# Performance work log

Measured on AMD Instinct MI355X. Metric: run time of the kernel, lower is better.

Reference implementation:

```python
import jax, jax.numpy as jnp
import numpy as np
from math import comb

G, NPG, D = 32, 128, 128   # graphs, nodes-per-graph, hidden dim
N = G * NPG                # 4096 nodes per side
E = 65536                  # edges per side (avg degree 16)
K = 6                      # Bernstein order (bern_k)
S, DCONV, DTR = 16, 4, 8   # mamba d_state, d_conv, dt_rank
HE = 27
SIGMAS = [1.0, 10.0, 100.0, 1000.0, 10000.0]


def _leaky(x, s=0.02):
    return jnp.where(x >= 0, x, s * x)


def _bnorm(x, g, b, eps=1e-5):
    m = jnp.mean(x, axis=0)
    v = jnp.var(x, axis=0)
    return (x - m) * jax.lax.rsqrt(v + eps) * g + b


def _bern_prop(x, src, dst, w, temp):
    # BernNet Bern_prop: Bernstein polynomial of sym-normalized Laplacian with weights relu(temp)
    n = x.shape[0]
    temp = jax.nn.relu(temp)
    deg = jax.ops.segment_sum(w, src, num_segments=n)
    dinv = jnp.where(deg > 0, 1.0 / jnp.sqrt(deg + 1e-12), 0.0)
    nw = (w * dinv[src] * dinv[dst])[:, None]
    adj = lambda v: jax.ops.segment_sum(nw * v[src], dst, num_segments=n)
    tmps = [x]
    xv = x
    for _ in range(K):
        xv = xv + adj(xv)          # (2I - L) v = v + A_norm v
        tmps.append(xv)
    out = (comb(K, 0) / 2 ** K) * temp[0] * tmps[K]
    for i in range(K):
        v = tmps[K - i - 1]
        for _ in range(i + 1):
            v = v - adj(v)         # L v = v - A_norm v
        out = out + (comb(K, i + 1) / 2 ** K) * temp[i + 1] * v
    return out


def _mamba(h, in_w, conv_w, conv_b, xproj_w, dt_w, dt_b, A_log, Dp, out_w):
    # Mamba block, d_model=D, expand=1 (d_inner=D), d_state=S, d_conv=DCONV
    Bb, L, _ = h.shape
    xq, z = jnp.split(h @ in_w, 2, axis=-1)             # [B,L,D] each
    xp = jnp.pad(xq, ((0, 0), (DCONV - 1, 0), (0, 0)))  # causal depthwise conv
    xc = conv_b + sum(xp[:, k:k + L, :] * conv_w[:, k] for k in range(DCONV))
    xc = jax.nn.silu(xc)
    dbl = xc @ xproj_w                                  # [B,L,DTR+2S]
    dt = jax.nn.softplus(dbl[..., :DTR] @ dt_w + dt_b)  # [B,L,D]
    Bm = dbl[..., DTR:DTR + S]
    Cm = dbl[..., DTR + S:]
    A = -jnp.exp(A_log)                                 # [D,S]
    dA = jnp.exp(dt[..., None] * A)                     # [B,L,D,S]
    dBx = dt[..., None] * Bm[:, :, None, :] * xc[..., None]

    def step(hs, ins):
        dA_t, dBx_t, C_t = ins
        hs = dA_t * hs + dBx_t
        return hs, jnp.einsum('bds,bs->bd', hs, C_t)

    h0 = jnp.zeros((Bb, D, S), h.dtype)
    _, ys = jax.lax.scan(step, h0, (jnp.swapaxes(dA, 0, 1),
                                    jnp.swapaxes(dBx, 0, 1),
                                    jnp.swapaxes(Cm, 0, 1)))
    y = jnp.swapaxes(ys, 0, 1) + xc * Dp
    return (y * jax.nn.silu(z)) @ out_w


def _xattn(q, k, v, mask):
    a = mask * (q @ k.T) - 1000.0 * (1.0 - mask)
    return jax.nn.softmax(a, axis=1) @ v


def setup_inputs():
    key = jax.random.key(0)
    ks = jax.random.split(key, 32)
    f = jnp.float32
    nrm = lambda k, shp, sc=1.0: jax.random.normal(k, shp, dtype=f) * sc
    h_lig = nrm(ks[0], (N, D), 0.5)
    h_rec = nrm(ks[1], (N, D), 0.5)
    x_lig = nrm(ks[2], (N, 3))
    x_rec = nrm(ks[3], (N, 3))
    he_1 = jax.random.uniform(ks[4], (E, HE), dtype=f)
    he_2 = jax.random.uniform(ks[5], (E, HE), dtype=f)
    g = (jnp.arange(E) // (E // G)).astype(jnp.int32)
    src1 = g * NPG + jax.random.randint(ks[6], (E,), 0, NPG, dtype=jnp.int32)
    dst1 = g * NPG + jax.random.randint(ks[7], (E,), 0, NPG, dtype=jnp.int32)
    src2 = g * NPG + jax.random.randint(ks[8], (E,), 0, NPG, dtype=jnp.int32)
    dst2 = g * NPG + jax.random.randint(ks[9], (E,), 0, NPG, dtype=jnp.int32)
    edge_index_1 = jnp.stack([src1, dst1])
    edge_index_2 = jnp.stack([src2, dst2])
    batch = (jnp.arange(N) // NPG).astype(jnp.int32)
    rng = np.random.default_rng(0)
    def mkperm(src):
        # lexsort([deg + noise, batch]) with batch as primary key
        deg = np.bincount(np.asarray(src), minlength=N).astype(np.float32)
        return jnp.asarray(np.lexsort((deg + rng.random(N).astype(np.float32),
                                       np.asarray(batch))).astype(np.int32))
    perm_1 = mkperm(src1)
    perm_2 = mkperm(src2)
    p = {}
    p['emlp_w1'] = nrm(ks[10], (32, D), 0.1)
    p['emlp_b1'] = jnp.zeros((D,), f)
    p['emlp_bn_g'] = jnp.ones((D,), f)
    p['emlp_bn_b'] = jnp.zeros((D,), f)
    p['emlp_w2'] = nrm(ks[11], (D, 1), 0.1)
    p['emlp_b2'] = jnp.zeros((1,), f)
    p['bern_temp'] = jnp.ones((K + 1,), f)
    p['m_in_w'] = nrm(ks[12], (D, 2 * D), 0.05)
    p['m_conv_w'] = nrm(ks[13], (D, DCONV), 0.2)
    p['m_conv_b'] = jnp.zeros((D,), f)
    p['m_xproj_w'] = nrm(ks[14], (D, DTR + 2 * S), 0.05)
    p['m_dt_w'] = nrm(ks[15], (DTR, D), 0.2)
    p['m_dt_b'] = jnp.full((D,), -4.0, f)
    p['m_A_log'] = jnp.log(jnp.broadcast_to(jnp.arange(1, S + 1, dtype=f), (D, S)))
    p['m_D'] = jnp.ones((D,), f)
    p['m_out_w'] = nrm(ks[16], (D, D), 0.05)
    p['q_w'] = nrm(ks[17], (D, D), 0.05)
    p['k_w'] = nrm(ks[18], (D, D), 0.05)
    p['v_w'] = nrm(ks[19], (D, D), 0.05)
    p['bn1_g'] = jnp.ones((D,), f)
    p['bn1_b'] = jnp.zeros((D,), f)
    p['bn2_g'] = jnp.ones((D,), f)
    p['bn2_b'] = jnp.zeros((D,), f)
    p['ff_w1'] = nrm(ks[20], (D, 2 * D), 0.05)
    p['ff_b1'] = jnp.zeros((2 * D,), f)
    p['ff_w2'] = nrm(ks[21], (2 * D, D), 0.05)
    p['ff_b2'] = jnp.zeros((D,), f)
    return dict(h_lig=h_lig, h_rec=h_rec, x_lig=x_lig, x_rec=x_rec,
                he_1=he_1, he_2=he_2, **p,
                edge_index_1=edge_index_1, edge_index_2=edge_index_2,
                batch_1=batch, batch_2=batch, perm_1=perm_1, perm_2=perm_2)


def reference(h_lig, h_rec, x_lig, x_rec, he_1, he_2,
              emlp_w1, emlp_b1, emlp_bn_g, emlp_bn_b, emlp_w2, emlp_b2,
              bern_temp, m_in_w, m_conv_w, m_conv_b, m_xproj_w, m_dt_w,
              m_dt_b, m_A_log, m_D, m_out_w, q_w, k_w, v_w,
              bn1_g, bn1_b, bn2_g, bn2_b, ff_w1, ff_b1, ff_w2, ff_b2,
              edge_index_1, edge_index_2, batch_1, batch_2, perm_1, perm_2):

    def side(h, x, he, ei, perm):
        src, dst = ei[0], ei[1]
        d2 = jnp.sum((x[src] - x[dst]) ** 2, axis=1, keepdims=True)
        ew = jnp.concatenate([jnp.exp(-d2 / s) for s in SIGMAS], axis=1)  # [E,5]
        t = _leaky(jnp.concatenate([ew, he], axis=1) @ emlp_w1 + emlp_b1)
        t = _bnorm(t, emlp_bn_g, emlp_bn_b)
        w = jax.nn.relu(t @ emlp_w2 + emlp_b2)[:, 0]                      # [E]
        h_local = _bern_prop(h, src, dst, w, bern_temp)
        inv = jnp.argsort(perm)
        hd = h[perm].reshape(G, NPG, D)   # uniform graph sizes -> exact dense batch
        ha = _mamba(hd, m_in_w, m_conv_w, m_conv_b, m_xproj_w, m_dt_w,
                    m_dt_b, m_A_log, m_D, m_out_w).reshape(N, D)[inv]
        return _bnorm(h + h_local + ha, bn1_g, bn1_b)

    hl = side(h_lig, x_lig, he_1, edge_index_1, perm_1)
    hr = side(h_rec, x_rec, he_2, edge_index_2, perm_2)
    mask = (batch_1[:, None] == batch_2[None, :]).astype(hl.dtype)
    cl = _xattn(_leaky(hl @ q_w), _leaky(hr @ k_w), hr @ v_w, mask)
    cr = _xattn(_leaky(hr @ q_w), _leaky(hl @ k_w), hl @ v_w, mask.T)
    hl = hl + cl
    hr = hr + cr
    ff = lambda h: jax.nn.relu(h @ ff_w1 + ff_b1) @ ff_w2 + ff_b2
    hl = _bnorm(hl + ff(hl), bn2_g, bn2_b)
    hr = _bnorm(hr + ff(hr), bn2_g, bn2_b)
    return hl, hr
```

## Files before the change

### kernel.cpp

```cpp
#include <hip/hip_runtime.h>
#include <math.h>

#define G_    32
#define NPG_  128
#define D_    128
#define N_    4096
#define E_    65536
#define ND_   (N_*D_)

#define W_OFF     0
#define DEG_OFF   65536
#define STATS_OFF 69632
#define BUF0      71680
#define HL_OFF    (BUF0 + 0*ND_)
#define HA_OFF    (BUF0 + 1*ND_)
#define X1_OFF    (BUF0 + 2*ND_)
#define HMID_OFF  (BUF0 + 3*ND_)
#define XC_OFF    (BUF0 + 4*ND_)
#define DTB_OFF   (BUF0 + 5*ND_)
#define YB_OFF    (BUF0 + 6*ND_)
#define XZ_OFF    (BUF0 + 7*ND_)
#define DBL_OFF   (BUF0 + 9*ND_)
#define SS_       ((size_t)(DBL_OFF + N_*40))

__device__ __forceinline__ float leakyf(float x){ return x >= 0.f ? x : 0.02f*x; }
__device__ __forceinline__ float siluf (float x){ return x / (1.f + expf(-x)); }

__device__ __forceinline__ void edge_feat(const float* __restrict__ x,
                                          const float* __restrict__ he,
                                          const int* __restrict__ ei,
                                          int e, float* feat, int& sN, int& dN)
{
  sN = ei[e]; dN = ei[E_ + e];
  float dx = x[sN*3+0]-x[dN*3+0];
  float dy = x[sN*3+1]-x[dN*3+1];
  float dz = x[sN*3+2]-x[dN*3+2];
  float d2 = dx*dx + dy*dy + dz*dz;
  feat[0] = expf(-d2/1.f);
  feat[1] = expf(-d2/10.f);
  feat[2] = expf(-d2/100.f);
  feat[3] = expf(-d2/1000.f);
  feat[4] = expf(-d2/10000.f);
#pragma unroll
  for (int j = 0; j < 27; ++j) feat[5+j] = he[(size_t)e*27 + j];
}

__global__ __launch_bounds__(256)
void edge_stats_kernel(const float* __restrict__ xl, const float* __restrict__ xr,
                       const float* __restrict__ hel, const float* __restrict__ her,
                       const int* __restrict__ ei1, const int* __restrict__ ei2,
                       const float* __restrict__ w1, const float* __restrict__ b1,
                       float* __restrict__ ws)
{
  int side = blockIdx.y;
  const float* x  = side ? xr  : xl;
  const float* he = side ? her : hel;
  const int*   ei = side ? ei2 : ei1;
  float* stats = ws + (size_t)side*SS_ + STATS_OFF;
  __shared__ float featl[256*36];
  __shared__ float csum[2][128], cssq[2][128];
  int tid = threadIdx.x;
  {
    int sN, dN; float feat[32];
    edge_feat(x, he, ei, blockIdx.x*256 + tid, feat, sN, dN);
#pragma unroll
    for (int j4 = 0; j4 < 8; ++j4)
      *(float4*)&featl[tid*36 + j4*4] = *(float4*)&feat[j4*4];
  }
  int c = tid & 127, hh = tid >> 7;
  float w1c[32];
#pragma unroll
  for (int j = 0; j < 32; ++j) w1c[j] = w1[j*128 + c];
  float b1c = b1[c];
  __syncthreads();
  float s1 = 0.f, s2 = 0.f;
  for (int e = 0; e < 128; ++e) {
    const float* f = &featl[(hh*128 + e)*36];
    float acc = b1c;
#pragma unroll
    for (int j4 = 0; j4 < 8; ++j4) {
      float4 f4 = *(const float4*)&f[j4*4];
      acc += f4.x*w1c[j4*4] + f4.y*w1c[j4*4+1] + f4.z*w1c[j4*4+2] + f4.w*w1c[j4*4+3];
    }
    float t = leakyf(acc);
    s1 += t; s2 += t*t;
  }
  csum[hh][c] = s1; cssq[hh][c] = s2;
  __syncthreads();
  if (tid < 128) {
    atomicAdd(&stats[tid],     csum[0][tid] + csum[1][tid]);
    atomicAdd(&stats[128+tid], cssq[0][tid] + cssq[1][tid]);
  }
}

__global__ void edge_finalize_kernel(const float* __restrict__ g_, const float* __restrict__ b_,
                                     const float* __restrict__ w2, const float* __restrict__ b2,
                                     float* __restrict__ ws)
{
  int side = blockIdx.y;
  float* stats = ws + (size_t)side*SS_ + STATS_OFF;
  __shared__ float red[128];
  int c = threadIdx.x;
  const float invE = 1.f/(float)E_;
  float mean = stats[c]*invE;
  float var  = fmaxf(stats[128+c]*invE - mean*mean, 0.f);
  float scale = rsqrtf(var + 1e-5f) * g_[c];
  stats[256+c] = scale * w2[c];
  red[c] = (b_[c] - mean*scale) * w2[c];
  __syncthreads();
  for (int off = 64; off; off >>= 1) { if (c < off) red[c] += red[c+off]; __syncthreads(); }
  if (c == 0) stats[384] = red[0] + b2[0];
}

__global__ __launch_bounds__(256)
void edge_w_kernel(const float* __restrict__ xl, const float* __restrict__ xr,
                   const float* __restrict__ hel, const float* __restrict__ her,
                   const int* __restrict__ ei1, const int* __restrict__ ei2,
                   const float* __restrict__ w1, const float* __restrict__ b1,
                   float* __restrict__ ws)
{
  int side = blockIdx.y;
  const float* x  = side ? xr  : xl;
  const float* he = side ? her : hel;
  const int*   ei = side ? ei2 : ei1;
  float* base = ws + (size_t)side*SS_;
  const float* stats = base + STATS_OFF;
  float* wbuf = base + W_OFF;
  float* deg  = base + DEG_OFF;
  __shared__ float w1t[128*32];
  __shared__ float b1l[128], all_[128];
  int tid = threadIdx.x;
  for (int i = tid; i < 4096; i += 256) {
    int j = i & 31, c = i >> 5;
    w1t[c*32 + j] = w1[j*128 + c];
  }
  if (tid < 128) { b1l[tid] = b1[tid]; all_[tid] = stats[256+tid]; }
  __syncthreads();
  int e = blockIdx.x*256 + tid;
  int sN, dN; float feat[32];
  edge_feat(x, he, ei, e, feat, sN, dN);
  float accw = stats[384];
  for (int c = 0; c < 128; ++c) {
    float acc = b1l[c];
#pragma unroll
    for (int j4 = 0; j4 < 8; ++j4) {
      float4 w4 = *(const float4*)&w1t[c*32 + j4*4];
      acc += feat[j4*4]*w4.x + feat[j4*4+1]*w4.y + feat[j4*4+2]*w4.z + feat[j4*4+3]*w4.w;
    }
    accw += leakyf(acc)*all_[c];
  }
  float w = fmaxf(accw, 0.f);
  wbuf[e] = w;
  atomicAdd(&deg[sN], w);
}

__global__ __launch_bounds__(256)
void bern_horner_kernel(const float* __restrict__ hl_in, const float* __restrict__ hr_in,
                        const int* __restrict__ ei1, const int* __restrict__ ei2,
                        const float* __restrict__ bern_temp, float* __restrict__ ws)
{
  int side = blockIdx.y;
  int g  = blockIdx.x >> 2;
  int d0 = (blockIdx.x & 3) * 32;
  const float* h  = side ? hr_in : hl_in;
  const int*   ei = side ? ei2 : ei1;
  float* base = ws + (size_t)side*SS_;
  const float* wbuf = base + W_OFF;
  const float* deg  = base + DEG_OFF;
  float* hloc = base + HL_OFF;

  __shared__ float A[128*132];
  __shared__ float v[128*32];
  int tid = threadIdx.x;
  for (int i = tid; i < 128*132; i += 256) A[i] = 0.f;

  const float btab[7][7] = {
    { 1,  6, 15,  20, 15,  6,  1},
    { 1,  4,  5,   0, -5, -4, -1},
    { 1,  2, -1,  -4, -1,  2,  1},
    { 1,  0, -3,   0,  3,  0, -1},
    { 1, -2, -1,   4, -1, -2,  1},
    { 1, -4,  5,   0, -5,  4, -1},
    { 1, -6, 15, -20, 15, -6,  1}};
  const float comb6[7] = {1,6,15,20,15,6,1};
  float a[7];
#pragma unroll
  for (int m = 0; m < 7; ++m) a[m] = 0.f;
#pragma unroll
  for (int j = 0; j < 7; ++j) {
    float tj = fmaxf(bern_temp[j], 0.f) * comb6[j] * (1.f/64.f);
#pragma unroll
    for (int m = 0; m < 7; ++m) a[m] += tj * btab[j][m];
  }
  __syncthreads();

  int ebase = g*2048, nbase = g*128;
  for (int i = tid; i < 2048; i += 256) {
    int e = ebase + i;
    int sN = ei[e], dN = ei[E_ + e];
    float ds_ = deg[sN], dd_ = deg[dN];
    float aa = ds_ > 0.f ? rsqrtf(ds_ + 1e-12f) : 0.f;
    float bb = dd_ > 0.f ? rsqrtf(dd_ + 1e-12f) : 0.f;
    atomicAdd(&A[(dN - nbase)*132 + (sN - nbase)], wbuf[e]*aa*bb);
  }

  const int db = (tid & 7)*4;
  const int rb = (tid >> 3)*4;
  float hreg[4][4], r[4][4], t[4][4];
#pragma unroll
  for (int i = 0; i < 4; ++i) {
    float4 h4 = *(const float4*)&h[(size_t)(nbase + rb + i)*128 + d0 + db];
    hreg[i][0]=h4.x; hreg[i][1]=h4.y; hreg[i][2]=h4.z; hreg[i][3]=h4.w;
#pragma unroll
    for (int jj = 0; jj < 4; ++jj) r[i][jj] = a[6]*hreg[i][jj];
  }

  for (int step = 5; step >= 0; --step) {
    __syncthreads();
#pragma unroll
    for (int i = 0; i < 4; ++i)
      *(float4*)&v[(rb+i)*32 + db] = make_float4(r[i][0], r[i][1], r[i][2], r[i][3]);
    __syncthreads();
#pragma unroll
    for (int i = 0; i < 4; ++i)
#pragma unroll
      for (int jj = 0; jj < 4; ++jj) t[i][jj] = 0.f;
    for (int k = 0; k < 128; k += 4) {
      float4 V0 = *(const float4*)&v[(k+0)*32 + db];
      float4 V1 = *(const float4*)&v[(k+1)*32 + db];
      float4 V2 = *(const float4*)&v[(k+2)*32 + db];
      float4 V3 = *(const float4*)&v[(k+3)*32 + db];
#pragma unroll
      for (int i = 0; i < 4; ++i) {
        float4 A4 = *(const float4*)&A[(rb+i)*132 + k];
        t[i][0] += A4.x*V0.x + A4.y*V1.x + A4.z*V2.x + A4.w*V3.x;
        t[i][1] += A4.x*V0.y + A4.y*V1.y + A4.z*V2.y + A4.w*V3.y;
        t[i][2] += A4.x*V0.z + A4.y*V1.z + A4.z*V2.z + A4.w*V3.z;
        t[i][3] += A4.x*V0.w + A4.y*V1.w + A4.z*V2.w + A4.w*V3.w;
      }
    }
    float ak = a[step];
#pragma unroll
    for (int i = 0; i < 4; ++i)
#pragma unroll
      for (int jj = 0; jj < 4; ++jj) r[i][jj] = t[i][jj] + ak*hreg[i][jj];
  }

#pragma unroll
  for (int i = 0; i < 4; ++i)
    *(float4*)&hloc[(size_t)(nbase + rb + i)*128 + d0 + db] =
        make_float4(r[i][0], r[i][1], r[i][2], r[i][3]);
}

template<int K, int NC, int TC, int CSPLIT, int ACT, int GATHER, int SCATTER, int ADDC, int BIAS>
__global__ __launch_bounds__(256)
void gemm_kernel(const float* __restrict__ A0, const float* __restrict__ A1, int lda,
                 const float* __restrict__ W, const float* __restrict__ bias,
                 float* __restrict__ C0, float* __restrict__ C1, int ldc,
                 const int* __restrict__ idx0, const int* __restrict__ idx1,
                 const float* __restrict__ add0, const float* __restrict__ add1)
{
  int side = blockIdx.y;
  const float* A = side ? A1 : A0;
  float* C = side ? C1 : C0;
  const int* idx = side ? idx1 : idx0;
  const float* addsrc = side ? add1 : add0;
  constexpr int RPT = TC/8;
  constexpr int CLEN = NC/CSPLIT;
  __shared__ float Alds[32][K];
  __shared__ float Wlds[K][TC];
  const int tid = threadIdx.x;
  const int r0 = (blockIdx.x / CSPLIT) * 32;
  const int cbase = (blockIdx.x % CSPLIT) * CLEN;
  for (int i = tid*4; i < 32*K; i += 1024) {
    int r = i / K, k = i % K;
    int row = GATHER ? idx[r0 + r] : (r0 + r);
    *(float4*)&Alds[r][k] = *(const float4*)&A[(size_t)row*lda + k];
  }
  for (int c0 = cbase; c0 < cbase + CLEN; c0 += TC) {
    __syncthreads();
    for (int i = tid*4; i < K*TC; i += 1024) {
      int k = i / TC, c = i % TC;
      if (c0 + c < NC) *(float4*)&Wlds[k][c] = *(const float4*)&W[k*NC + c0 + c];
      else             *(float4*)&Wlds[k][c] = make_float4(0.f,0.f,0.f,0.f);
    }
    __syncthreads();
    const int cl = tid % TC;
    const int rsub = (tid / TC) * RPT;
    float accv[RPT];
#pragma unroll
    for (int j = 0; j < RPT; ++j) accv[j] = 0.f;
    for (int k = 0; k < K; k += 4) {
      float w0 = Wlds[k][cl], w1v = Wlds[k+1][cl], w2v = Wlds[k+2][cl], w3v = Wlds[k+3][cl];
#pragma unroll
      for (int j = 0; j < RPT; ++j) {
        float4 a4 = *(const float4*)&Alds[rsub+j][k];
        accv[j] += a4.x*w0 + a4.y*w1v + a4.z*w2v + a4.w*w3v;
      }
    }
    int c = c0 + cl;
    if (c < NC) {
#pragma unroll
      for (int j = 0; j < RPT; ++j) {
        int row  = r0 + rsub + j;
        int orow = SCATTER ? idx[row] : row;
        float vv = accv[j];
        if (BIAS)     vv += bias[c];
        if (ACT == 1) vv = leakyf(vv);
        if (ACT == 2) vv = fmaxf(vv, 0.f);
        if (ADDC)     vv += addsrc[(size_t)orow*ldc + c];
        C[(size_t)orow*ldc + c] = vv;
      }
    }
  }
}

__global__ __launch_bounds__(256)
void qkv_kernel(const float* __restrict__ qw, const float* __restrict__ kw,
                const float* __restrict__ vw, float* __restrict__ ws)
{
  int side = blockIdx.y;
  int mat  = blockIdx.z;
  float* base = ws + (size_t)side*SS_;
  const float* A = base + HMID_OFF;
  const float* W = mat == 0 ? qw : (mat == 1 ? kw : vw);
  float* C = base + (mat == 0 ? XC_OFF : (mat == 1 ? DTB_OFF : YB_OFF));
  __shared__ float Alds[32][128];
  __shared__ float Wlds[128][64];
  const int tid = threadIdx.x;
  const int r0 = (blockIdx.x >> 1) * 32;
  const int c0 = (blockIdx.x & 1) * 64;
  for (int i = tid*4; i < 32*128; i += 1024)
    *(float4*)&Alds[i>>7][i&127] = *(const float4*)&A[(size_t)(r0 + (i>>7))*128 + (i&127)];
  for (int i = tid*4; i < 128*64; i += 1024)
    *(float4*)&Wlds[i>>6][i&63] = *(const float4*)&W[(i>>6)*128 + c0 + (i&63)];
  __syncthreads();
  const int cl = tid & 63;
  const int rsub = (tid >> 6) * 8;
  float accv[8];
#pragma unroll
  for (int j = 0; j < 8; ++j) accv[j] = 0.f;
  for (int k = 0; k < 128; k += 4) {
    float w0 = Wlds[k][cl], w1v = Wlds[k+1][cl], w2v = Wlds[k+2][cl], w3v = Wlds[k+3][cl];
#pragma unroll
    for (int j = 0; j < 8; ++j) {
      float4 a4 = *(const float4*)&Alds[rsub+j][k];
      accv[j] += a4.x*w0 + a4.y*w1v + a4.z*w2v + a4.w*w3v;
    }
  }
#pragma unroll
  for (int j = 0; j < 8; ++j) {
    float vv = accv[j];
    if (mat < 2) vv = leakyf(vv);
    C[(size_t)(r0 + rsub + j)*128 + c0 + cl] = vv;
  }
}

__global__ __launch_bounds__(256)
void conv_kernel(const float* __restrict__ cw, const float* __restrict__ cb, float* __restrict__ ws)
{
  int side = blockIdx.y;
  float* base = ws + (size_t)side*SS_;
  const float* xz = base + XZ_OFF;
  float* xc = base + XC_OFF;
  int i = blockIdx.x*256 + threadIdx.x;
  int j = i >> 7, d = i & 127;
  int l = j & 127;
  float a = cb[d];
#pragma unroll
  for (int k = 0; k < 4; ++k) {
    int ll = l - 3 + k;
    if (ll >= 0) a += xz[(size_t)(j-3+k)*256 + d] * cw[d*4 + k];
  }
  xc[i] = siluf(a);
}

__global__ __launch_bounds__(256)
void scan_kernel(const float* __restrict__ A_log, const float* __restrict__ Dp,
                 const float* __restrict__ dtw, const float* __restrict__ dtbias,
                 float* __restrict__ ws)
{
  int side = blockIdx.z;
  int g  = blockIdx.x;
  int d0 = blockIdx.y * 16;
  float* base = ws + (size_t)side*SS_;
  const float* dbl = base + DBL_OFF;
  const float* xcb = base + XC_OFF;
  float* xz = base + XZ_OFF;

  __shared__ float ldbl[128][40];
  __shared__ float lxc[128][16];
  __shared__ float ldt[128][16];
  __shared__ float lz[128][16];
  __shared__ float ly[128][16];
  __shared__ float ltw[8][16];
  __shared__ float ltb[16];

  int tid = threadIdx.x;
  int rowbase = g*128;
  if (tid < 128)      ltw[tid>>4][tid&15] = dtw[(tid>>4)*128 + d0 + (tid&15)];
  else if (tid < 144) ltb[tid-128] = dtbias[d0 + (tid-128)];
  for (int i = tid; i < 128*40; i += 256)
    ((float*)ldbl)[i] = dbl[(size_t)rowbase*40 + i];
  for (int i = tid; i < 2048; i += 256) {
    int l = i >> 4, dd = i & 15;
    lxc[l][dd] = xcb[(size_t)(rowbase+l)*128 + d0 + dd];
    lz[l][dd]  = xz[(size_t)(rowbase+l)*256 + 128 + d0 + dd];
  }
  __syncthreads();
  for (int i = tid; i < 2048; i += 256) {
    int l = i >> 4, dd = i & 15;
    float a = ltb[dd];
#pragma unroll
    for (int k = 0; k < 8; ++k) a += ldbl[l][k]*ltw[k][dd];
    ldt[l][dd] = a > 20.f ? a : log1pf(expf(a));
  }
  __syncthreads();

  int s = tid & 15, dl = (tid >> 4) & 15;
  float Ac  = -expf(A_log[(d0+dl)*16 + s]);
  float dpv = Dp[d0+dl];
  float hsv = 0.f;
  for (int l = 0; l < 128; ++l) {
    float dtv = ldt[l][dl];
    float xcv = lxc[l][dl];
    float Bv  = ldbl[l][8+s];
    float Cv  = ldbl[l][24+s];
    hsv = expf(dtv*Ac)*hsv + (dtv*xcv)*Bv;
    float val = hsv*Cv;
    val += __shfl_xor(val, 1, 16);
    val += __shfl_xor(val, 2, 16);
    val += __shfl_xor(val, 4, 16);
    val += __shfl_xor(val, 8, 16);
    if (s == 0) ly[l][dl] = val + xcv*dpv;
  }
  __syncthreads();
  for (int i = tid; i < 2048; i += 256) {
    int l = i >> 4, dd = i & 15;
    float y = ly[l][dd];
    float z = lz[l][dd];
    xz[(size_t)(rowbase+l)*256 + d0 + dd] = y * siluf(z);
  }
}

__global__ __launch_bounds__(256)
void stats_kernel(const float* __restrict__ hl_in, const float* __restrict__ hr_in,
                  float* __restrict__ ws, int mode, int statsoff)
{
  int side = blockIdx.y;
  float* base = ws + (size_t)side*SS_;
  const float* h    = side ? hr_in : hl_in;
  const float* hloc = base + HL_OFF;
  const float* ha   = base + HA_OFF;
  float* x1 = base + X1_OFF;
  float* stats = base + STATS_OFF + statsoff;
  int tid = threadIdx.x;
  int c = tid & 127;
  float s1 = 0.f, s2 = 0.f;
  for (int it = 0; it < 16; ++it) {
    int r = blockIdx.x*32 + (tid >> 7) + it*2;
    size_t i = (size_t)r*128 + c;
    float v;
    if (mode == 0) { v = h[i] + hloc[i] + ha[i]; x1[i] = v; }
    else           { v = ha[i]; }
    s1 += v; s2 += v*v;
  }
  __shared__ float red[256];
  red[tid] = s1; __syncthreads();
  if (tid < 128) atomicAdd(&stats[tid], red[tid] + red[tid+128]);
  __syncthreads();
  red[tid] = s2; __syncthreads();
  if (tid < 128) atomicAdd(&stats[128+tid], red[tid] + red[tid+128]);
}

__global__ void bn_finalize_kernel(const float* __restrict__ g_, const float* __restrict__ b_,
                                   float* __restrict__ ws, int statsoff, float invM)
{
  int side = blockIdx.y;
  float* stats = ws + (size_t)side*SS_ + STATS_OFF + statsoff;
  int c = threadIdx.x;
  float mean = stats[c]*invM;
  float var  = fmaxf(stats[128+c]*invM - mean*mean, 0.f);
  float scale = rsqrtf(var + 1e-5f) * g_[c];
  stats[256+c] = scale;
  stats[384+c] = b_[c] - mean*scale;
}

__global__ __launch_bounds__(256)
void bn_apply_kernel(float* __restrict__ ws, float* __restrict__ dout,
                     int srcoff, int dstoff, int statsoff, int to_dout)
{
  int side = blockIdx.y;
  float* base = ws + (size_t)side*SS_;
  const float* src = base + srcoff;
  const float* stats = base + STATS_OFF + statsoff;
  float* dst = to_dout ? (dout + (size_t)side*ND_) : (base + dstoff);
  size_t i = (size_t)blockIdx.x*256 + threadIdx.x;
  int c = (int)(i & 127);
  dst[i] = src[i]*stats[256+c] + stats[384+c];
}

__global__ __launch_bounds__(256)
void attn_kernel(float* __restrict__ ws)
{
  int dir = blockIdx.z;
  int g   = blockIdx.x;
  int rt  = blockIdx.y;
  float* baseq = ws + (size_t)dir*SS_;
  float* basek = ws + (size_t)(1-dir)*SS_;
  const float* qb = baseq + XC_OFF;
  const float* kb = basek + DTB_OFF;
  const float* vb = basek + YB_OFF;
  const float* hm = baseq + HMID_OFF;
  float* h2 = baseq + X1_OFF;
  __shared__ float kT[128*129];
  __shared__ float sp[32*128];
  int tid = threadIdx.x;
  for (int i = tid; i < 16384; i += 256) {
    int n = i >> 7, d = i & 127;
    kT[d*129 + n] = kb[(size_t)(g*128+n)*128 + d];
  }
  __syncthreads();
  int wv = tid >> 6, lane = tid & 63;
  for (int rl = wv; rl < 32; rl += 4) {
    int r = g*128 + rt*32 + rl;
    const float* qrow = qb + (size_t)r*128;
    float a0 = 0.f, a1 = 0.f;
    for (int d = 0; d < 128; ++d) {
      float qv = qrow[d];
      a0 += qv * kT[d*129 + lane];
      a1 += qv * kT[d*129 + 64 + lane];
    }
    float m = fmaxf(a0, a1);
#pragma unroll
    for (int off = 32; off; off >>= 1) m = fmaxf(m, __shfl_xor(m, off));
    float p0 = expf(a0 - m), p1 = expf(a1 - m);
    float ssum = p0 + p1;
#pragma unroll
    for (int off = 32; off; off >>= 1) ssum += __shfl_xor(ssum, off);
    float inv = 1.f/ssum;
    sp[rl*128 + lane]      = p0*inv;
    sp[rl*128 + 64 + lane] = p1*inv;
  }
  __syncthreads();
  for (int i = tid; i < 16384; i += 256) {
    int n = i >> 7, d = i & 127;
    kT[n*129 + d] = vb[(size_t)(g*128+n)*128 + d];
  }
  __syncthreads();
  for (int rl = wv; rl < 32; rl += 4) {
    int r = g*128 + rt*32 + rl;
    float a0 = 0.f, a1 = 0.f;
    const float* prow = sp + rl*128;
    for (int c = 0; c < 128; ++c) {
      float p = prow[c];
      a0 += p * kT[c*129 + lane];
      a1 += p * kT[c*129 + 64 + lane];
    }
    size_t o = (size_t)r*128;
    h2[o + lane]      = hm[o + lane]      + a0;
    h2[o + 64 + lane] = hm[o + 64 + lane] + a1;
  }
}

extern "C" void kernel_launch(void* const* d_in, const int* in_sizes, int n_in,
                              void* d_out, int out_size, void* d_ws, size_t ws_size,
                              hipStream_t stream)
{
  const float* h_lig     = (const float*)d_in[0];
  const float* h_rec     = (const float*)d_in[1];
  const float* x_lig     = (const float*)d_in[2];
  const float* x_rec     = (const float*)d_in[3];
  const float* he_1      = (const float*)d_in[4];
  const float* he_2      = (const float*)d_in[5];
  const float* emlp_w1   = (const float*)d_in[6];
  const float* emlp_b1   = (const float*)d_in[7];
  const float* emlp_bn_g = (const float*)d_in[8];
  const float* emlp_bn_b = (const float*)d_in[9];
  const float* emlp_w2   = (const float*)d_in[10];
  const float* emlp_b2   = (const float*)d_in[11];
  const float* bern_temp = (const float*)d_in[12];
  const float* m_in_w    = (const float*)d_in[13];
  const float* m_conv_w  = (const float*)d_in[14];
  const float* m_conv_b  = (const float*)d_in[15];
  const float* m_xproj_w = (const float*)d_in[16];
  const float* m_dt_w    = (const float*)d_in[17];
  const float* m_dt_b    = (const float*)d_in[18];
  const float* m_A_log   = (const float*)d_in[19];
  const float* m_D       = (const float*)d_in[20];
  const float* m_out_w   = (const float*)d_in[21];
  const float* q_w       = (const float*)d_in[22];
  const float* k_w       = (const float*)d_in[23];
  const float* v_w       = (const float*)d_in[24];
  const float* bn1_g     = (const float*)d_in[25];
  const float* bn1_b     = (const float*)d_in[26];
  const float* bn2_g     = (const float*)d_in[27];
  const float* bn2_b     = (const float*)d_in[28];
  const float* ff_w1     = (const float*)d_in[29];
  const float* ff_b1     = (const float*)d_in[30];
  const float* ff_w2     = (const float*)d_in[31];
  const float* ff_b2     = (const float*)d_in[32];
  const int*   ei1       = (const int*)d_in[33];
  const int*   ei2       = (const int*)d_in[34];
  const int*   perm1     = (const int*)d_in[37];
  const int*   perm2     = (const int*)d_in[38];

  float* ws   = (float*)d_ws;
  float* dout = (float*)d_out;

#define B0(off) (ws + (size_t)(off))
#define B1(off) (ws + SS_ + (size_t)(off))

  for (int s = 0; s < 2; ++s)
    hipMemsetAsync((char*)d_ws + ((size_t)s*SS_ + DEG_OFF)*sizeof(float), 0,
                   (N_ + 2048)*sizeof(float), stream);

  edge_stats_kernel<<<dim3(256,2), 256, 0, stream>>>(x_lig,x_rec,he_1,he_2,ei1,ei2,emlp_w1,emlp_b1,ws);
  edge_finalize_kernel<<<dim3(1,2), 128, 0, stream>>>(emlp_bn_g,emlp_bn_b,emlp_w2,emlp_b2,ws);
  edge_w_kernel<<<dim3(256,2), 256, 0, stream>>>(x_lig,x_rec,he_1,he_2,ei1,ei2,emlp_w1,emlp_b1,ws);

  bern_horner_kernel<<<dim3(G_*4,2), 256, 0, stream>>>(h_lig,h_rec,ei1,ei2,bern_temp,ws);

  gemm_kernel<128,256,64,4,0,1,0,0,0><<<dim3(512,2),256,0,stream>>>(
      h_lig,h_rec,128, m_in_w,nullptr, B0(XZ_OFF),B1(XZ_OFF),256, perm1,perm2, nullptr,nullptr);
  conv_kernel<<<dim3(2048,2), 256, 0, stream>>>(m_conv_w,m_conv_b,ws);
  gemm_kernel<128,40,64,1,0,0,0,0,0><<<dim3(128,2),256,0,stream>>>(
      B0(XC_OFF),B1(XC_OFF),128, m_xproj_w,nullptr, B0(DBL_OFF),B1(DBL_OFF),40, nullptr,nullptr, nullptr,nullptr);
  scan_kernel<<<dim3(32,8,2), 256, 0, stream>>>(m_A_log,m_D,m_dt_w,m_dt_b,ws);
  gemm_kernel<128,128,64,2,0,0,1,0,0><<<dim3(256,2),256,0,stream>>>(
      B0(XZ_OFF),B1(XZ_OFF),256, m_out_w,nullptr, B0(HA_OFF),B1(HA_OFF),128, perm1,perm2, nullptr,nullptr);

  stats_kernel<<<dim3(128,2), 256, 0, stream>>>(h_lig,h_rec,ws,0,512);
  bn_finalize_kernel<<<dim3(1,2), 128, 0, stream>>>(bn1_g,bn1_b,ws,512,1.f/(float)N_);
  bn_apply_kernel<<<dim3(2048,2), 256, 0, stream>>>(ws,dout,X1_OFF,HMID_OFF,512,0);

  qkv_kernel<<<dim3(256,2,3), 256, 0, stream>>>(q_w,k_w,v_w,ws);
  attn_kernel<<<dim3(32,4,2), 256, 0, stream>>>(ws);

  gemm_kernel<128,256,64,4,2,0,0,0,1><<<dim3(512,2),256,0,stream>>>(
      B0(X1_OFF),B1(X1_OFF),128, ff_w1,ff_b1, B0(XZ_OFF),B1(XZ_OFF),256, nullptr,nullptr, nullptr,nullptr);
  gemm_kernel<256,128,32,4,0,0,0,1,1><<<dim3(512,2),256,0,stream>>>(
      B0(XZ_OFF),B1(XZ_OFF),256, ff_w2,ff_b2, B0(HA_OFF),B1(HA_OFF),128, nullptr,nullptr, B0(X1_OFF),B1(X1_OFF));
  stats_kernel<<<dim3(128,2), 256, 0, stream>>>(h_lig,h_rec,ws,1,1024);
  bn_finalize_kernel<<<dim3(1,2), 128, 0, stream>>>(bn2_g,bn2_b,ws,1024,1.f/(float)N_);
  bn_apply_kernel<<<dim3(2048,2), 256, 0, stream>>>(ws,dout,HA_OFF,0,1024,1);
}
```

Before: 484.0 us.

## Register-tile cross-attention kernel with 4x4 outputs per thread and float4 LDS

Rewrites the per-graph cross-attention kernel so each thread computes a 4x4 output tile in registers, with Q staged in shared memory and K/V/P read as float4. The softmax normalisation is deferred to the final output scaling, and global loads are vectorised. This is meant to cut shared-memory traffic and instruction count in the two small matmuls, at the cost of more registers and more LDS use per block.

```diff
diff --git a/kernel.cpp b/kernel.cpp
--- a/kernel.cpp
+++ b/kernel.cpp
@@ -513,53 +513,114 @@
   const float* vb = basek + YB_OFF;
   const float* hm = baseq + HMID_OFF;
   float* h2 = baseq + X1_OFF;
-  __shared__ float kT[128*129];
-  __shared__ float sp[32*128];
-  int tid = threadIdx.x;
-  for (int i = tid; i < 16384; i += 256) {
-    int n = i >> 7, d = i & 127;
-    kT[d*129 + n] = kb[(size_t)(g*128+n)*128 + d];
-  }
-  __syncthreads();
-  int wv = tid >> 6, lane = tid & 63;
-  for (int rl = wv; rl < 32; rl += 4) {
-    int r = g*128 + rt*32 + rl;
-    const float* qrow = qb + (size_t)r*128;
-    float a0 = 0.f, a1 = 0.f;
-    for (int d = 0; d < 128; ++d) {
-      float qv = qrow[d];
-      a0 += qv * kT[d*129 + lane];
-      a1 += qv * kT[d*129 + 64 + lane];
-    }
-    float m = fmaxf(a0, a1);
-#pragma unroll
-    for (int off = 32; off; off >>= 1) m = fmaxf(m, __shfl_xor(m, off));
-    float p0 = expf(a0 - m), p1 = expf(a1 - m);
-    float ssum = p0 + p1;
-#pragma unroll
-    for (int off = 32; off; off >>= 1) ssum += __shfl_xor(ssum, off);
-    float inv = 1.f/ssum;
-    sp[rl*128 + lane]      = p0*inv;
-    sp[rl*128 + 64 + lane] = p1*inv;
-  }
-  __syncthreads();
-  for (int i = tid; i < 16384; i += 256) {
-    int n = i >> 7, d = i & 127;
-    kT[n*129 + d] = vb[(size_t)(g*128+n)*128 + d];
-  }
-  __syncthreads();
-  for (int rl = wv; rl < 32; rl += 4) {
-    int r = g*128 + rt*32 + rl;
-    float a0 = 0.f, a1 = 0.f;
-    const float* prow = sp + rl*128;
-    for (int c = 0; c < 128; ++c) {
-      float p = prow[c];
-      a0 += p * kT[c*129 + lane];
-      a1 += p * kT[c*129 + 64 + lane];
-    }
-    size_t o = (size_t)r*128;
-    h2[o + lane]      = hm[o + lane]      + a0;
-    h2[o + 64 + lane] = hm[o + 64 + lane] + a1;
+
+  __shared__ float KT[128][132];
+  __shared__ float Qs[32][132];
+  __shared__ float sp[32][132];
+
+  const int tid = threadIdx.x;
+  const int cl  = tid & 31;
+  const int r0  = (tid >> 5) * 4;
+  const int c0  = cl * 4;
+  const int rowg = g*128 + rt*32;
+
+  {
+    const float* qsrc = qb + (size_t)rowg*128;
+    for (int i = tid; i < 32*32; i += 256) {
+      int r = i >> 5, d4 = i & 31;
+      *(float4*)&Qs[r][d4*4] = *(const float4*)&qsrc[(size_t)r*128 + d4*4];
+    }
+  }
+  {
+    const float* ksrc = kb + (size_t)(g*128)*128;
+    for (int i = tid; i < 128*32; i += 256) {
+      int d4 = i >> 7, n = i & 127;
+      float4 k4 = *(const float4*)&ksrc[(size_t)n*128 + d4*4];
+      KT[d4*4+0][n] = k4.x;
+      KT[d4*4+1][n] = k4.y;
+      KT[d4*4+2][n] = k4.z;
+      KT[d4*4+3][n] = k4.w;
+    }
+  }
+  __syncthreads();
+
+  float acc[4][4];
+#pragma unroll
+  for (int i = 0; i < 4; ++i)
+#pragma unroll
+    for (int j = 0; j < 4; ++j) acc[i][j] = 0.f;
+
+  for (int d = 0; d < 128; d += 4) {
+    float4 k0 = *(const float4*)&KT[d+0][c0];
+    float4 k1 = *(const float4*)&KT[d+1][c0];
+    float4 k2 = *(const float4*)&KT[d+2][c0];
+    float4 k3 = *(const float4*)&KT[d+3][c0];
+#pragma unroll
+    for (int i = 0; i < 4; ++i) {
+      float4 q4 = *(const float4*)&Qs[r0+i][d];
+      acc[i][0] += q4.x*k0.x + q4.y*k1.x + q4.z*k2.x + q4.w*k3.x;
+      acc[i][1] += q4.x*k0.y + q4.y*k1.y + q4.z*k2.y + q4.w*k3.y;
+      acc[i][2] += q4.x*k0.z + q4.y*k1.z + q4.z*k2.z + q4.w*k3.z;
+      acc[i][3] += q4.x*k0.w + q4.y*k1.w + q4.z*k2.w + q4.w*k3.w;
+    }
+  }
+
+  float inv[4];
+#pragma unroll
+  for (int i = 0; i < 4; ++i) {
+    float m = fmaxf(fmaxf(acc[i][0], acc[i][1]), fmaxf(acc[i][2], acc[i][3]));
+#pragma unroll
+    for (int off = 1; off < 32; off <<= 1) m = fmaxf(m, __shfl_xor(m, off, 32));
+    float p0 = expf(acc[i][0]-m), p1 = expf(acc[i][1]-m);
+    float p2 = expf(acc[i][2]-m), p3 = expf(acc[i][3]-m);
+    float s = p0 + p1 + p2 + p3;
+#pragma unroll
+    for (int off = 1; off < 32; off <<= 1) s += __shfl_xor(s, off, 32);
+    inv[i] = 1.f/s;
+    *(float4*)&sp[r0+i][c0] = make_float4(p0, p1, p2, p3);
+  }
+  __syncthreads();
+
+  {
+    const float* vsrc = vb + (size_t)(g*128)*128;
+    for (int i = tid; i < 128*32; i += 256) {
+      int n = i >> 5, d4 = i & 31;
+      *(float4*)&KT[n][d4*4] = *(const float4*)&vsrc[(size_t)n*128 + d4*4];
+    }
+  }
+  __syncthreads();
+
+  float o[4][4];
+#pragma unroll
+  for (int i = 0; i < 4; ++i)
+#pragma unroll
+    for (int j = 0; j < 4; ++j) o[i][j] = 0.f;
+
+  for (int n = 0; n < 128; n += 4) {
+    float4 v0 = *(const float4*)&KT[n+0][c0];
+    float4 v1 = *(const float4*)&KT[n+1][c0];
+    float4 v2 = *(const float4*)&KT[n+2][c0];
+    float4 v3 = *(const float4*)&KT[n+3][c0];
+#pragma unroll
+    for (int i = 0; i < 4; ++i) {
+      float4 p4 = *(const float4*)&sp[r0+i][n];
+      o[i][0] += p4.x*v0.x + p4.y*v1.x + p4.z*v2.x + p4.w*v3.x;
+      o[i][1] += p4.x*v0.y + p4.y*v1.y + p4.z*v2.y + p4.w*v3.y;
+      o[i][2] += p4.x*v0.z + p4.y*v1.z + p4.z*v2.z + p4.w*v3.z;
+      o[i][3] += p4.x*v0.w + p4.y*v1.w + p4.z*v2.w + p4.w*v3.w;
+    }
+  }
+
+#pragma unroll
+  for (int i = 0; i < 4; ++i) {
+    size_t off = (size_t)(rowg + r0 + i)*128 + c0;
+    float4 hm4 = *(const float4*)&hm[off];
+    float4 r4;
+    r4.x = hm4.x + o[i][0]*inv[i];
+    r4.y = hm4.y + o[i][1]*inv[i];
+    r4.z = hm4.z + o[i][2]*inv[i];
+    r4.w = hm4.w + o[i][3]*inv[i];
+    *(float4*)&h2[off] = r4;
   }
 }
 
```

Result: faster. 458.1 us (-5.4%).
